# Performance work log

Measured on AMD Instinct MI355X. Metric: run time of the kernel, lower is better.

Reference implementation:

```python
import jax, jax.numpy as jnp
import numpy as np

N_NODES = 100000
N_EDGES = 1250000
D_IN = 64
D_OUT = 64


def setup_inputs() -> dict:
    key = jax.random.key(0)
    k_h, k_e, k_src, k_dst, k_w, k_b = jax.random.split(key, 6)
    h = jax.random.normal(k_h, (N_NODES, D_IN), dtype=jnp.float32)
    e = jax.random.normal(k_e, (N_EDGES, 1), dtype=jnp.float32)
    src = jax.random.randint(k_src, (N_EDGES,), 0, N_NODES, dtype=jnp.int64)
    dst = jax.random.randint(k_dst, (N_EDGES,), 0, N_NODES, dtype=jnp.int64)
    W = jax.random.normal(k_w, (D_OUT, D_IN), dtype=jnp.float32) / np.sqrt(D_IN)
    b = jax.random.normal(k_b, (D_OUT,), dtype=jnp.float32) * 0.01
    return {"h": h, "e": e, "src": src, "dst": dst, "W": W, "b": b}


def reference(h, e, src, dst, W, b):
    # u_mul_e: gather source node features and multiply by edge features [E,1] -> [E,D]
    m = h[src] * e
    # fn.sum('m','ft'): scatter-add messages into destination nodes -> [N,D]
    ft = jax.ops.segment_sum(m, dst, num_segments=N_NODES)
    # nn.Linear(input_dim, output_dim)
    return ft @ W.T + b
```

## Files before the change

### kernel.cpp

```cpp
#include <hip/hip_runtime.h>

#define N_NODES 100000
#define N_EDGES 1250000
#define D 64
#define BUCKET_BITS 6
#define BUCKET_SZ 64
#define NBUCK 1563
#define CAP 1024
#define EPT 16
#define EPB (EPT * 256)
#define BIN_BLOCKS ((N_EDGES + EPB - 1) / EPB)
#define TR_BLOCKS ((N_NODES + 63) / 64)
#define FUSED_BLOCKS (TR_BLOCKS + BIN_BLOCKS)


typedef __attribute__((ext_vector_type(8))) short bf16x8;
typedef __attribute__((ext_vector_type(4))) float f32x4;

__device__ __forceinline__ unsigned bf16_rne(float x) {
    unsigned u = __float_as_uint(x);
    return (u + 0x7FFFu + ((u >> 16) & 1u)) >> 16;
}
__device__ __forceinline__ float bf16_to_f(unsigned short v) {
    return __uint_as_float(((unsigned)v) << 16);
}

__device__ __forceinline__ void bf16_split(float x, short& hi, short& lo) {
    unsigned hb = bf16_rne(x);
    float fh = __uint_as_float(hb << 16);
    hi = (short)hb;
    lo = (short)bf16_rne(x - fh);
}

__global__ __launch_bounds__(256) void transform_bin_kernel(const float* __restrict__ h,
                                                            const float* __restrict__ W,
                                                            unsigned short* __restrict__ g16,
                                                            const int* __restrict__ src,
                                                            const int* __restrict__ dst,
                                                            const float* __restrict__ e,
                                                            int* __restrict__ gcursor,
                                                            int2* __restrict__ packed) {
    __shared__ unsigned short sh[64 * D];
    __shared__ int lhist[NBUCK];

    int t = threadIdx.x;

    if (blockIdx.x < TR_BLOCKS) {
        int lane = t & 63;
        int w = t >> 6;
        int li = lane & 15;
        int lg = lane >> 4;
        int nodebase = blockIdx.x * 64 + w * 16;

        bf16x8 bhi[4][2], blo[4][2];
#pragma unroll
        for (int nt = 0; nt < 4; ++nt) {
#pragma unroll
            for (int kk = 0; kk < 2; ++kk) {
                const float* wp = W + (nt * 16 + li) * D + kk * 32 + lg * 8;
                float4 w0 = *(const float4*)wp;
                float4 w1 = *(const float4*)(wp + 4);
                float v[8] = {w0.x, w0.y, w0.z, w0.w, w1.x, w1.y, w1.z, w1.w};
                bf16x8 h8, l8;
#pragma unroll
                for (int q = 0; q < 8; ++q) { short a, b; bf16_split(v[q], a, b); h8[q] = a; l8[q] = b; }
                bhi[nt][kk] = h8;
                blo[nt][kk] = l8;
            }
        }

        int arow = nodebase + li;
        if (arow > N_NODES - 1) arow = N_NODES - 1;
        bf16x8 ahi[2], alo[2];
#pragma unroll
        for (int kk = 0; kk < 2; ++kk) {
            const float* hp = h + (long)arow * D + kk * 32 + lg * 8;
            float4 h0 = *(const float4*)hp;
            float4 h1 = *(const float4*)(hp + 4);
            float v[8] = {h0.x, h0.y, h0.z, h0.w, h1.x, h1.y, h1.z, h1.w};
            bf16x8 h8, l8;
#pragma unroll
            for (int q = 0; q < 8; ++q) { short a, b; bf16_split(v[q], a, b); h8[q] = a; l8[q] = b; }
            ahi[kk] = h8;
            alo[kk] = l8;
        }

        f32x4 acc[4];
#pragma unroll
        for (int nt = 0; nt < 4; ++nt) acc[nt] = (f32x4){0.f, 0.f, 0.f, 0.f};
#pragma unroll
        for (int kk = 0; kk < 2; ++kk) {
#pragma unroll
            for (int nt = 0; nt < 4; ++nt) {
                acc[nt] = __builtin_amdgcn_mfma_f32_16x16x32_bf16(ahi[kk], bhi[nt][kk], acc[nt], 0, 0, 0);
                acc[nt] = __builtin_amdgcn_mfma_f32_16x16x32_bf16(ahi[kk], blo[nt][kk], acc[nt], 0, 0, 0);
                acc[nt] = __builtin_amdgcn_mfma_f32_16x16x32_bf16(alo[kk], bhi[nt][kk], acc[nt], 0, 0, 0);
            }
        }

#pragma unroll
        for (int nt = 0; nt < 4; ++nt) {
#pragma unroll
            for (int r = 0; r < 4; ++r) {
                sh[(w * 16 + lg * 4 + r) * D + nt * 16 + li] = (unsigned short)bf16_rne(acc[nt][r]);
            }
        }
        __syncthreads();

        const uint4* s4 = (const uint4*)sh;
        uint4* g4 = (uint4*)(g16 + (long)blockIdx.x * 64 * D);
#pragma unroll
        for (int i = t; i < 512; i += 256) {
            int n = blockIdx.x * 64 + (i >> 3);
            if (n < N_NODES) g4[i] = s4[i];
        }
    } else {
        for (int j = t; j < NBUCK; j += 256) lhist[j] = 0;
        __syncthreads();

        int b[EPT], r[EPT], sv[EPT];
        float ev[EPT];
        int base = (blockIdx.x - TR_BLOCKS) * EPB;
#pragma unroll
        for (int j = 0; j < EPT; ++j) {
            int i = base + j * 256 + t;
            b[j] = -1;
            if (i < N_EDGES) {
                int d = dst[i];
                b[j] = d >> BUCKET_BITS;
                sv[j] = src[i] | ((d & (BUCKET_SZ - 1)) << 20);
                ev[j] = e[i];
                r[j] = atomicAdd(&lhist[b[j]], 1);
            }
        }
        __syncthreads();

        for (int x = t; x < NBUCK; x += 256) {
            int c = lhist[x];
            lhist[x] = (c > 0) ? atomicAdd(&gcursor[x], c) : 0;
        }
        __syncthreads();

#pragma unroll
        for (int j = 0; j < EPT; ++j) {
            if (b[j] >= 0) {
                int pos = lhist[b[j]] + r[j];
                if (pos < CAP) packed[b[j] * CAP + pos] = make_int2(sv[j], __float_as_int(ev[j]));
            }
        }
    }
}

__global__ __launch_bounds__(512) void gather_bucket_kernel(const unsigned short* __restrict__ g16,
                                                            const int2* __restrict__ packed,
                                                            const int* __restrict__ gcursor,
                                                            const float* __restrict__ bias,
                                                            float* __restrict__ out) {
    __shared__ int2 eds[CAP];
    __shared__ int nhist[BUCKET_SZ];
    __shared__ int nbase[BUCKET_SZ];
    __shared__ int ncur[BUCKET_SZ];

    int t = threadIdx.x;
    int bk = blockIdx.x;
    int start = bk * CAP;
    int cnt = gcursor[bk];
    if (cnt > CAP) cnt = CAP;

    if (t < BUCKET_SZ) nhist[t] = 0;
    __syncthreads();

    int2 pa = make_int2(0, 0), pb = pa;
    bool va = t < cnt, vb = t + 512 < cnt;
    if (va) pa = packed[start + t];
    if (vb) pb = packed[start + t + 512];
    if (va) atomicAdd(&nhist[(pa.x >> 20) & (BUCKET_SZ - 1)], 1);
    if (vb) atomicAdd(&nhist[(pb.x >> 20) & (BUCKET_SZ - 1)], 1);
    __syncthreads();

    if (t < BUCKET_SZ) {
        int c = nhist[t];
        int v = c;
#pragma unroll
        for (int off = 1; off < BUCKET_SZ; off <<= 1) {
            int x = __shfl_up(v, off, 64);
            if (t >= off) v += x;
        }
        nbase[t] = v - c;
        ncur[t] = v - c;
    }
    __syncthreads();

    if (va) { int dl = (pa.x >> 20) & (BUCKET_SZ - 1); eds[atomicAdd(&ncur[dl], 1)] = pa; }
    if (vb) { int dl = (pb.x >> 20) & (BUCKET_SZ - 1); eds[atomicAdd(&ncur[dl], 1)] = pb; }
    __syncthreads();

    int w = t >> 6;
    int lane = t & 63;
    float bv = bias[lane];
    for (int jj = 0; jj < 8; ++jj) {
        int n = w * 8 + jj;
        int gn = bk * BUCKET_SZ + n;
        int s = nbase[n];
        int c = nhist[n];
        float acc = bv;
        int k = 0;
        for (; k + 8 <= c; k += 8) {
            int2 q0 = eds[s + k + 0], q1 = eds[s + k + 1];
            int2 q2 = eds[s + k + 2], q3 = eds[s + k + 3];
            int2 q4 = eds[s + k + 4], q5 = eds[s + k + 5];
            int2 q6 = eds[s + k + 6], q7 = eds[s + k + 7];
            float g0 = bf16_to_f(g16[(long)(q0.x & 0xFFFFF) * D + lane]);
            float g1 = bf16_to_f(g16[(long)(q1.x & 0xFFFFF) * D + lane]);
            float g2 = bf16_to_f(g16[(long)(q2.x & 0xFFFFF) * D + lane]);
            float g3 = bf16_to_f(g16[(long)(q3.x & 0xFFFFF) * D + lane]);
            float g4 = bf16_to_f(g16[(long)(q4.x & 0xFFFFF) * D + lane]);
            float g5 = bf16_to_f(g16[(long)(q5.x & 0xFFFFF) * D + lane]);
            float g6 = bf16_to_f(g16[(long)(q6.x & 0xFFFFF) * D + lane]);
            float g7 = bf16_to_f(g16[(long)(q7.x & 0xFFFFF) * D + lane]);
            acc += __int_as_float(q0.y) * g0;
            acc += __int_as_float(q1.y) * g1;
            acc += __int_as_float(q2.y) * g2;
            acc += __int_as_float(q3.y) * g3;
            acc += __int_as_float(q4.y) * g4;
            acc += __int_as_float(q5.y) * g5;
            acc += __int_as_float(q6.y) * g6;
            acc += __int_as_float(q7.y) * g7;
        }
        if (k + 4 <= c) {
            int2 q0 = eds[s + k + 0], q1 = eds[s + k + 1];
            int2 q2 = eds[s + k + 2], q3 = eds[s + k + 3];
            float g0 = bf16_to_f(g16[(long)(q0.x & 0xFFFFF) * D + lane]);
            float g1 = bf16_to_f(g16[(long)(q1.x & 0xFFFFF) * D + lane]);
            float g2 = bf16_to_f(g16[(long)(q2.x & 0xFFFFF) * D + lane]);
            float g3 = bf16_to_f(g16[(long)(q3.x & 0xFFFFF) * D + lane]);
            acc += __int_as_float(q0.y) * g0;
            acc += __int_as_float(q1.y) * g1;
            acc += __int_as_float(q2.y) * g2;
            acc += __int_as_float(q3.y) * g3;
            k += 4;
        }
        for (; k < c; ++k) {
            int2 q = eds[s + k];
            acc += __int_as_float(q.y) * bf16_to_f(g16[(long)(q.x & 0xFFFFF) * D + lane]);
        }
        if (gn < N_NODES) out[(long)gn * D + lane] = acc;
    }
}

extern "C" void kernel_launch(void* const* d_in, const int* in_sizes, int n_in,
                              void* d_out, int out_size, void* d_ws, size_t ws_size,
                              hipStream_t stream) {
    const float* h   = (const float*)d_in[0];
    const float* e   = (const float*)d_in[1];
    const int*   src = (const int*)d_in[2];
    const int*   dst = (const int*)d_in[3];
    const float* W   = (const float*)d_in[4];
    const float* b   = (const float*)d_in[5];
    float* out = (float*)d_out;

    char* ws = (char*)d_ws;
    int2*           packed  = (int2*)          (ws);
    int*            gcursor = (int*)           (ws + 12804096);
    unsigned short* g16     = (unsigned short*)(ws + 12810368);

    hipMemsetAsync(gcursor, 0, NBUCK * sizeof(int), stream);

    transform_bin_kernel<<<FUSED_BLOCKS, 256, 0, stream>>>(h, W, g16, src, dst, e, gcursor, packed);

    gather_bucket_kernel<<<NBUCK, 512, 0, stream>>>(g16, packed, gcursor, b, out);
}
```

Before: 157.9 us.

## Merge transform and edge binning into every block with direct global atomics

Every block now computes its 64-node transform and then bins 800 edges, where before the work was split between two kinds of block. Binning drops the shared-memory histogram and uses one global atomicAdd per edge on the bucket cursor. Per-block register use drops because the W hi/lo fragments are built per k-step, and a min-blocks launch bound of 4 is added. The aim is better balance and occupancy, at the cost of far more global atomic contention on 1563 counters.

Result: slower. 320.4 us (+102.9%).

```diff
diff --git a/kernel.cpp b/kernel.cpp
--- a/kernel.cpp
+++ b/kernel.cpp
@@ -7,11 +7,8 @@
 #define BUCKET_SZ 64
 #define NBUCK 1563
 #define CAP 1024
-#define EPT 16
-#define EPB (EPT * 256)
-#define BIN_BLOCKS ((N_EDGES + EPB - 1) / EPB)
 #define TR_BLOCKS ((N_NODES + 63) / 64)
-#define FUSED_BLOCKS (TR_BLOCKS + BIN_BLOCKS)
+#define EPS 800
 
 
 typedef __attribute__((ext_vector_type(8))) short bf16x8;
@@ -32,122 +29,105 @@
     lo = (short)bf16_rne(x - fh);
 }
 
-__global__ __launch_bounds__(256) void transform_bin_kernel(const float* __restrict__ h,
-                                                            const float* __restrict__ W,
-                                                            unsigned short* __restrict__ g16,
-                                                            const int* __restrict__ src,
-                                                            const int* __restrict__ dst,
-                                                            const float* __restrict__ e,
-                                                            int* __restrict__ gcursor,
-                                                            int2* __restrict__ packed) {
+__global__ __launch_bounds__(256, 4) void transform_bin_kernel(const float* __restrict__ h,
+                                                               const float* __restrict__ W,
+                                                               unsigned short* __restrict__ g16,
+                                                               const int* __restrict__ src,
+                                                               const int* __restrict__ dst,
+                                                               const float* __restrict__ e,
+                                                               int* __restrict__ gcursor,
+                                                               int2* __restrict__ packed) {
     __shared__ unsigned short sh[64 * D];
-    __shared__ int lhist[NBUCK];
 
     int t = threadIdx.x;
-
-    if (blockIdx.x < TR_BLOCKS) {
-        int lane = t & 63;
-        int w = t >> 6;
-        int li = lane & 15;
-        int lg = lane >> 4;
-        int nodebase = blockIdx.x * 64 + w * 16;
-
-        bf16x8 bhi[4][2], blo[4][2];
+    int bx = blockIdx.x;
+    int lane = t & 63;
+    int w = t >> 6;
+    int li = lane & 15;
+    int lg = lane >> 4;
+    int nodebase = bx * 64 + w * 16;
+
+    int arow = nodebase + li;
+    if (arow > N_NODES - 1) arow = N_NODES - 1;
+
+    f32x4 acc[4];
+#pragma unroll
+    for (int nt = 0; nt < 4; ++nt) acc[nt] = (f32x4){0.f, 0.f, 0.f, 0.f};
+
+#pragma unroll
+    for (int kk = 0; kk < 2; ++kk) {
+        const float* hp = h + (long)arow * D + kk * 32 + lg * 8;
+        float4 h0 = *(const float4*)hp;
+        float4 h1 = *(const float4*)(hp + 4);
+        float av[8] = {h0.x, h0.y, h0.z, h0.w, h1.x, h1.y, h1.z, h1.w};
+        bf16x8 ahi, alo;
+#pragma unroll
+        for (int q = 0; q < 8; ++q) { short a, b; bf16_split(av[q], a, b); ahi[q] = a; alo[q] = b; }
+
 #pragma unroll
         for (int nt = 0; nt < 4; ++nt) {
-#pragma unroll
-            for (int kk = 0; kk < 2; ++kk) {
-                const float* wp = W + (nt * 16 + li) * D + kk * 32 + lg * 8;
-                float4 w0 = *(const float4*)wp;
-                float4 w1 = *(const float4*)(wp + 4);
-                float v[8] = {w0.x, w0.y, w0.z, w0.w, w1.x, w1.y, w1.z, w1.w};
-                bf16x8 h8, l8;
-#pragma unroll
-                for (int q = 0; q < 8; ++q) { short a, b; bf16_split(v[q], a, b); h8[q] = a; l8[q] = b; }
-                bhi[nt][kk] = h8;
-                blo[nt][kk] = l8;
-            }
-        }
-
-        int arow = nodebase + li;
-        if (arow > N_NODES - 1) arow = N_NODES - 1;
-        bf16x8 ahi[2], alo[2];
-#pragma unroll
-        for (int kk = 0; kk < 2; ++kk) {
-            const float* hp = h + (long)arow * D + kk * 32 + lg * 8;
-            float4 h0 = *(const float4*)hp;
-            float4 h1 = *(const float4*)(hp + 4);
-            float v[8] = {h0.x, h0.y, h0.z, h0.w, h1.x, h1.y, h1.z, h1.w};
-            bf16x8 h8, l8;
-#pragma unroll
-            for (int q = 0; q < 8; ++q) { short a, b; bf16_split(v[q], a, b); h8[q] = a; l8[q] = b; }
-            ahi[kk] = h8;
-            alo[kk] = l8;
-        }
-
-        f32x4 acc[4];
-#pragma unroll
-        for (int nt = 0; nt < 4; ++nt) acc[nt] = (f32x4){0.f, 0.f, 0.f, 0.f};
-#pragma unroll
-        for (int kk = 0; kk < 2; ++kk) {
-#pragma unroll
-            for (int nt = 0; nt < 4; ++nt) {
-                acc[nt] = __builtin_amdgcn_mfma_f32_16x16x32_bf16(ahi[kk], bhi[nt][kk], acc[nt], 0, 0, 0);
-                acc[nt] = __builtin_amdgcn_mfma_f32_16x16x32_bf16(ahi[kk], blo[nt][kk], acc[nt], 0, 0, 0);
-                acc[nt] = __builtin_amdgcn_mfma_f32_16x16x32_bf16(alo[kk], bhi[nt][kk], acc[nt], 0, 0, 0);
-            }
-        }
-
-#pragma unroll
-        for (int nt = 0; nt < 4; ++nt) {
-#pragma unroll
-            for (int r = 0; r < 4; ++r) {
-                sh[(w * 16 + lg * 4 + r) * D + nt * 16 + li] = (unsigned short)bf16_rne(acc[nt][r]);
-            }
-        }
-        __syncthreads();
-
-        const uint4* s4 = (const uint4*)sh;
-        uint4* g4 = (uint4*)(g16 + (long)blockIdx.x * 64 * D);
-#pragma unroll
-        for (int i = t; i < 512; i += 256) {
-            int n = blockIdx.x * 64 + (i >> 3);
-            if (n < N_NODES) g4[i] = s4[i];
-        }
-    } else {
-        for (int j = t; j < NBUCK; j += 256) lhist[j] = 0;
-        __syncthreads();
-
-        int b[EPT], r[EPT], sv[EPT];
-        float ev[EPT];
-        int base = (blockIdx.x - TR_BLOCKS) * EPB;
-#pragma unroll
-        for (int j = 0; j < EPT; ++j) {
-            int i = base + j * 256 + t;
-            b[j] = -1;
-            if (i < N_EDGES) {
-                int d = dst[i];
-                b[j] = d >> BUCKET_BITS;
-                sv[j] = src[i] | ((d & (BUCKET_SZ - 1)) << 20);
-                ev[j] = e[i];
-                r[j] = atomicAdd(&lhist[b[j]], 1);
-            }
-        }
-        __syncthreads();
-
-        for (int x = t; x < NBUCK; x += 256) {
-            int c = lhist[x];
-            lhist[x] = (c > 0) ? atomicAdd(&gcursor[x], c) : 0;
-        }
-        __syncthreads();
-
-#pragma unroll
-        for (int j = 0; j < EPT; ++j) {
-            if (b[j] >= 0) {
-                int pos = lhist[b[j]] + r[j];
-                if (pos < CAP) packed[b[j] * CAP + pos] = make_int2(sv[j], __float_as_int(ev[j]));
-            }
-        }
+            const float* wp = W + (nt * 16 + li) * D + kk * 32 + lg * 8;
+            float4 w0 = *(const float4*)wp;
+            float4 w1 = *(const float4*)(wp + 4);
+            float bv[8] = {w0.x, w0.y, w0.z, w0.w, w1.x, w1.y, w1.z, w1.w};
+            bf16x8 bhi, blo;
+#pragma unroll
+            for (int q = 0; q < 8; ++q) { short a, b; bf16_split(bv[q], a, b); bhi[q] = a; blo[q] = b; }
+
+            acc[nt] = __builtin_amdgcn_mfma_f32_16x16x32_bf16(ahi, bhi, acc[nt], 0, 0, 0);
+            acc[nt] = __builtin_amdgcn_mfma_f32_16x16x32_bf16(ahi, blo, acc[nt], 0, 0, 0);
+            acc[nt] = __builtin_amdgcn_mfma_f32_16x16x32_bf16(alo, bhi, acc[nt], 0, 0, 0);
+        }
+    }
+
+#pragma unroll
+    for (int nt = 0; nt < 4; ++nt) {
+#pragma unroll
+        for (int r = 0; r < 4; ++r) {
+            sh[(w * 16 + lg * 4 + r) * D + nt * 16 + li] = (unsigned short)bf16_rne(acc[nt][r]);
+        }
+    }
+    __syncthreads();
+
+    const uint4* s4 = (const uint4*)sh;
+    uint4* g4 = (uint4*)(g16 + (long)bx * 64 * D);
+#pragma unroll
+    for (int i = t; i < 512; i += 256) {
+        int n = bx * 64 + (i >> 3);
+        if (n < N_NODES) g4[i] = s4[i];
+    }
+
+    int ebase = bx * EPS;
+    int i0 = ebase + t, i1 = i0 + 256, i2 = i0 + 512, i3 = i0 + 768;
+    int eend = ebase + EPS;
+    if (eend > N_EDGES) eend = N_EDGES;
+    bool v0 = i0 < eend, v1 = i1 < eend, v2 = i2 < eend, v3 = i3 < eend;
+    int d0 = 0, d1 = 0, d2 = 0, d3 = 0;
+    int s0 = 0, s1 = 0, s2 = 0, s3 = 0;
+    float e0 = 0.f, e1 = 0.f, e2 = 0.f, e3 = 0.f;
+    if (v0) { d0 = dst[i0]; s0 = src[i0]; e0 = e[i0]; }
+    if (v1) { d1 = dst[i1]; s1 = src[i1]; e1 = e[i1]; }
+    if (v2) { d2 = dst[i2]; s2 = src[i2]; e2 = e[i2]; }
+    if (v3) { d3 = dst[i3]; s3 = src[i3]; e3 = e[i3]; }
+    if (v0) {
+        int bk = d0 >> BUCKET_BITS;
+        int pos = atomicAdd(&gcursor[bk], 1);
+        if (pos < CAP) packed[bk * CAP + pos] = make_int2(s0 | ((d0 & (BUCKET_SZ - 1)) << 20), __float_as_int(e0));
+    }
+    if (v1) {
+        int bk = d1 >> BUCKET_BITS;
+        int pos = atomicAdd(&gcursor[bk], 1);
+        if (pos < CAP) packed[bk * CAP + pos] = make_int2(s1 | ((d1 & (BUCKET_SZ - 1)) << 20), __float_as_int(e1));
+    }
+    if (v2) {
+        int bk = d2 >> BUCKET_BITS;
+        int pos = atomicAdd(&gcursor[bk], 1);
+        if (pos < CAP) packed[bk * CAP + pos] = make_int2(s2 | ((d2 & (BUCKET_SZ - 1)) << 20), __float_as_int(e2));
+    }
+    if (v3) {
+        int bk = d3 >> BUCKET_BITS;
+        int pos = atomicAdd(&gcursor[bk], 1);
+        if (pos < CAP) packed[bk * CAP + pos] = make_int2(s3 | ((d3 & (BUCKET_SZ - 1)) << 20), __float_as_int(e3));
     }
 }
 
@@ -266,7 +246,7 @@
 
     hipMemsetAsync(gcursor, 0, NBUCK * sizeof(int), stream);
 
-    transform_bin_kernel<<<FUSED_BLOCKS, 256, 0, stream>>>(h, W, g16, src, dst, e, gcursor, packed);
+    transform_bin_kernel<<<TR_BLOCKS, 256, 0, stream>>>(h, W, g16, src, dst, e, gcursor, packed);
 
     gather_bucket_kernel<<<NBUCK, 512, 0, stream>>>(g16, packed, gcursor, b, out);
 }
```
